# Optimization experiments

Measured on AMD Instinct MI355X. Metric: run time of the kernel, lower is better.

## Reference

```python
import jax, jax.numpy as jnp
import numpy as np

CONF_THRES = 0.25
IOU_THRES = 0.45
MAX_DET = 300
MAX_WH = 4096.0  # class offset for class-aware (non-agnostic) NMS
B, N, NC = 16, 25200, 80


def setup_inputs() -> dict:
    key = jax.random.key(0)
    k1, k2 = jax.random.split(key)
    p = jax.random.uniform(k1, (B, N, 5 + NC), dtype=jnp.float32)
    # scale to realistic YOLO pixel-space xywh for a 640x640 image
    cx = p[..., 0] * 640.0
    cy = p[..., 1] * 640.0
    w = p[..., 2] * 96.0 + 4.0
    h = p[..., 3] * 96.0 + 4.0
    obj = p[..., 4]
    cls = p[..., 5:] * 0.9
    prediction = jnp.concatenate([jnp.stack([cx, cy, w, h, obj], axis=-1), cls], axis=-1)
    logits = jax.random.normal(k2, (B, N, NC), dtype=jnp.float32)
    return {"prediction": prediction, "logits": logits}


def xywh2xyxy(b):
    cx, cy, w, h = b[..., 0], b[..., 1], b[..., 2], b[..., 3]
    return jnp.stack([cx - w * 0.5, cy - h * 0.5, cx + w * 0.5, cy + h * 0.5], axis=-1)


def _iou_one_vs_all(box, boxes):
    # box: [4], boxes: [N,4] in xyxy
    lt = jnp.maximum(box[:2], boxes[:, :2])
    rb = jnp.minimum(box[2:], boxes[:, 2:])
    wh = jnp.clip(rb - lt, 0.0)
    inter = wh[:, 0] * wh[:, 1]
    a1 = (box[2] - box[0]) * (box[3] - box[1])
    a2 = (boxes[:, 2] - boxes[:, 0]) * (boxes[:, 3] - boxes[:, 1])
    return inter / (a1 + a2 - inter + 1e-9)


def _nms_image(x6, boxes_off, scores, log_):
    # greedy NMS, fixed MAX_DET iterations; suppressed/invalid scores are -1
    def step(s, _):
        best = jnp.argmax(s)
        keep = s[best] > 0.0
        iou = _iou_one_vs_all(boxes_off[best], boxes_off)
        s = jnp.where(iou > IOU_THRES, -1.0, s)  # also suppresses 'best' (IoU=1)
        return s, (best, keep)
    _, (idx, keep) = jax.lax.scan(step, scores, None, length=MAX_DET)
    km = keep.astype(x6.dtype)[:, None]
    dets = x6[idx] * km          # [MAX_DET, 6] zero-padded
    lg = log_[idx] * km          # [MAX_DET, 80]
    return dets, lg, keep


def reference(prediction, logits):
    obj = prediction[..., 4]                          # [B,N]
    cls_conf = prediction[..., 5:] * obj[..., None]   # x[:,5:] *= x[:,4:5]
    conf = jnp.max(cls_conf, axis=-1)                 # best class conf
    j = jnp.argmax(cls_conf, axis=-1)                 # best class index
    box = xywh2xyxy(prediction[..., :4])              # [B,N,4]
    valid = (obj > CONF_THRES) & (conf > CONF_THRES)
    scores = jnp.where(valid, conf, -1.0)
    boxes_off = box + (j.astype(box.dtype) * MAX_WH)[..., None]  # class-aware offset
    x6 = jnp.concatenate([box, conf[..., None], j.astype(box.dtype)[..., None]], axis=-1)
    dets, lg, keep = jax.vmap(_nms_image)(x6, boxes_off, scores, logits)
    return dets, lg, keep
```

## Files before the change

### kernel.cpp

```cpp
#include <hip/hip_runtime.h>
#include <cstdint>

#define BB 16
#define NN 25200
#define NCLS 80
#define ROW 85
#define MAXDET 300
#define HBINS 2048
#define CAP2 512
#define TGT 448
#define CONF_T 0.25f
#define IOU_T 0.45f
#define NT 1024

static const size_t OFF_SCR = 6451200;
static const size_t OFF_CLS = 8064000;

__global__ __launch_bounds__(64) void k_pre(const float* __restrict__ pred,
                                            float4* __restrict__ boxArr,
                                            float* __restrict__ scoreArr,
                                            unsigned* __restrict__ clsArr) {
    __shared__ float tile[64 * 85];
    int lane = threadIdx.x;
    int rowbase = blockIdx.x * 64;
    const float4* src = (const float4*)(pred + (size_t)rowbase * ROW);
    float4 r[21];
#pragma unroll
    for (int it = 0; it < 21; ++it) r[it] = src[it * 64 + lane];
    float tailv = pred[(size_t)rowbase * ROW + 5376 + lane];
#pragma unroll
    for (int it = 0; it < 21; ++it) *(float4*)&tile[(it * 64 + lane) * 4] = r[it];
    tile[5376 + lane] = tailv;
    __syncthreads();

    const float* row = &tile[lane * ROW];
    float cx = row[0], cy = row[1], w = row[2], h = row[3], obj = row[4];
    float best = __fmul_rn(row[5], obj);
    int bj = 0;
#pragma unroll 4
    for (int c = 1; c < NCLS; ++c) {
        float v = __fmul_rn(row[5 + c], obj);
        if (v > best) { best = v; bj = c; }
    }
    float hw = __fmul_rn(w, 0.5f), hh = __fmul_rn(h, 0.5f);
    float4 bx;
    bx.x = __fsub_rn(cx, hw);
    bx.y = __fsub_rn(cy, hh);
    bx.z = __fadd_rn(cx, hw);
    bx.w = __fadd_rn(cy, hh);
    bool valid = (obj > CONF_T) && (best > CONF_T);

    int i = rowbase + lane;
    boxArr[i] = bx;
    scoreArr[i] = valid ? best : -1.0f;
    clsArr[i] = (unsigned)bj;
}

__global__ __launch_bounds__(NT) void k_nms(const float4* __restrict__ boxArr,
                                            const unsigned* __restrict__ clsArr,
                                            const float* __restrict__ logits,
                                            const float* __restrict__ scoreArr,
                                            float* __restrict__ out) {
    __shared__ __align__(16) char smem[63792];
    float*    ls    = (float*)smem;
    int*      li    = (int*)(smem + 2048);
    int*      flags = (int*)(smem + 4096);
    unsigned* hist  = (unsigned*)(smem + 4112);
    unsigned* csum  = (unsigned*)(smem + 12304);
    unsigned long long* mask = (unsigned long long*)(smem + 4112);
    float4*   cbox  = (float4*)(smem + 36880);
    float4*   rawbox= (float4*)(smem + 45072);
    unsigned* ccls  = (unsigned*)(smem + 53264);
    float4*   rowbox= (float4*)(smem + 55312);
    float*    rowscore = (float*)(smem + 60112);
    unsigned* rowcls   = (unsigned*)(smem + 61312);
    unsigned long long* keepm = (unsigned long long*)(smem + 62512);
    unsigned* rowsrc   = (unsigned*)(smem + 62576);

    int b = blockIdx.x, tid = threadIdx.x;

    for (int k = tid; k < HBINS; k += NT) hist[k] = 0u;
    if (tid == 0) { flags[0] = 0; flags[1] = 0; }
    __syncthreads();

    float sreg[25];
#pragma unroll
    for (int t = 0; t < 25; ++t) {
        int n = tid + t * NT;
        float s = (n < NN) ? scoreArr[(size_t)b * NN + n] : -1.0f;
        sreg[t] = s;
        if (s > 0.0f) {
            unsigned key = (__float_as_uint(s) - 0x3E800000u) >> 13;
            if (key > HBINS - 1) key = HBINS - 1;
            atomicAdd(&hist[key], 1u);
        }
    }
    __syncthreads();

    if (tid < 256) {
        unsigned cs = 0;
#pragma unroll
        for (int t = 0; t < 8; ++t) cs += hist[tid * 8 + t];
        csum[tid] = cs;
    }
    __syncthreads();
    for (int off = 1; off < 256; off <<= 1) {
        unsigned v = 0, add = 0;
        if (tid < 256) {
            v = csum[tid];
            add = (tid + off < 256) ? csum[tid + off] : 0u;
        }
        __syncthreads();
        if (tid < 256) csum[tid] = v + add;
        __syncthreads();
    }
    if (tid < 256) {
        unsigned Sc = csum[tid];
        unsigned Sn = (tid < 255) ? csum[tid + 1] : 0u;
        if (Sc >= TGT && (tid == 255 || Sn < TGT)) {
            unsigned cum = Sn;
            int t = tid * 8;
            for (int k = tid * 8 + 7; k >= tid * 8; --k) {
                cum += hist[k];
                if (cum >= TGT) { t = k; break; }
            }
            flags[1] = t;
        }
    }
    __syncthreads();
    unsigned thr = (unsigned)flags[1];

#pragma unroll
    for (int t = 0; t < 25; ++t) {
        float s = sreg[t];
        if (s > 0.0f) {
            unsigned key = (__float_as_uint(s) - 0x3E800000u) >> 13;
            if (key > HBINS - 1) key = HBINS - 1;
            if (key >= thr) {
                int pos = atomicAdd(&flags[0], 1);
                if (pos < CAP2) { ls[pos] = s; li[pos] = tid + t * NT; }
            }
        }
    }
    __syncthreads();
    int c = min(flags[0], CAP2);
    for (int p = tid; p < CAP2; p += NT)
        if (p >= c) { ls[p] = -1e30f; li[p] = 0x7fffffff; }
    __syncthreads();

    for (int k = 2; k <= CAP2; k <<= 1) {
        for (int j = k >> 1; j > 0; j >>= 1) {
            for (int i = tid; i < CAP2; i += NT) {
                int ixj = i ^ j;
                if (ixj > i) {
                    float s1 = ls[i], s2 = ls[ixj];
                    int i1 = li[i], i2 = li[ixj];
                    bool before = (s1 > s2) || (s1 == s2 && i1 < i2);
                    bool sw = ((i & k) == 0) ? !before : before;
                    if (sw) { ls[i] = s2; ls[ixj] = s1; li[i] = i2; li[ixj] = i1; }
                }
            }
            __syncthreads();
        }
    }

    for (int p = tid; p < CAP2; p += NT) {
        if (p < c) {
            int n = li[p];
            float4 bb = boxArr[(size_t)b * NN + n];
            unsigned cl = clsArr[(size_t)b * NN + n];
            rawbox[p] = bb;
            float off = __fmul_rn((float)cl, 4096.0f);
            float4 ob;
            ob.x = __fadd_rn(bb.x, off);
            ob.y = __fadd_rn(bb.y, off);
            ob.z = __fadd_rn(bb.z, off);
            ob.w = __fadd_rn(bb.w, off);
            cbox[p] = ob;
            ccls[p] = cl;
        } else {
            rawbox[p] = make_float4(0.f, 0.f, 0.f, 0.f);
            cbox[p]   = make_float4(0.f, 0.f, 0.f, 0.f);
            ccls[p] = 0u;
        }
    }
    __syncthreads();

    for (int task = tid; task < CAP2 * 8; task += NT) {
        int i = task & (CAP2 - 1);
        int w = task >> 9;
        unsigned long long m = 0ULL;
        if (i < c) {
            float4 ci = cbox[i];
            float a1 = __fmul_rn(__fsub_rn(ci.z, ci.x), __fsub_rn(ci.w, ci.y));
#pragma unroll 4
            for (int jj = 0; jj < 64; ++jj) {
                float4 cj = cbox[w * 64 + jj];
                float ltx = fmaxf(ci.x, cj.x), lty = fmaxf(ci.y, cj.y);
                float rbx = fminf(ci.z, cj.z), rby = fminf(ci.w, cj.w);
                float ww = fmaxf(__fsub_rn(rbx, ltx), 0.0f);
                float hh = fmaxf(__fsub_rn(rby, lty), 0.0f);
                float inter = __fmul_rn(ww, hh);
                if (inter > 0.0f) {
                    float a2 = __fmul_rn(__fsub_rn(cj.z, cj.x), __fsub_rn(cj.w, cj.y));
                    float denom = __fadd_rn(__fsub_rn(__fadd_rn(a1, a2), inter), 1e-9f);
                    if (inter / denom > IOU_T) m |= (1ULL << jj);
                }
            }
        }
        mask[i * 8 + w] = m;
    }
    __syncthreads();

    if (tid < 64) {
        unsigned long long rem[8] = {0,0,0,0,0,0,0,0};
        unsigned long long kp[8]  = {0,0,0,0,0,0,0,0};
        int kept = 0;
        for (int p = 0; p < c && kept < MAXDET; ++p) {
            int w = p >> 6, bit = p & 63;
            if (!((rem[w] >> bit) & 1ULL)) {
                kp[w] |= (1ULL << bit);
                kept++;
#pragma unroll
                for (int q = 0; q < 8; ++q) rem[q] |= mask[p * 8 + q];
            }
        }
        if (tid == 0) {
            flags[2] = kept;
#pragma unroll
            for (int q = 0; q < 8; ++q) keepm[q] = kp[q];
        }
    }
    __syncthreads();
    int kept = flags[2];

    {
        unsigned long long km[8];
#pragma unroll
        for (int q = 0; q < 8; ++q) km[q] = keepm[q];
        for (int p = tid; p < c; p += NT) {
            int w = p >> 6, bit = p & 63;
            if ((km[w] >> bit) & 1ULL) {
                int rank = __popcll(km[w] & ((1ULL << bit) - 1ULL));
#pragma unroll
                for (int q = 0; q < 8; ++q) rank += (q < w) ? __popcll(km[q]) : 0;
                if (rank < MAXDET) {
                    rowbox[rank] = rawbox[p];
                    rowscore[rank] = ls[p];
                    rowcls[rank] = ccls[p];
                    rowsrc[rank] = (unsigned)li[p];
                }
            }
        }
    }
    __syncthreads();

    float* dets = out;
    float* lg   = out + (size_t)BB * MAXDET * 6;
    float* kpo  = lg  + (size_t)BB * MAXDET * NCLS;

    for (int i = tid; i < MAXDET * 6; i += NT) {
        int t = i / 6, col = i - t * 6;
        float v = 0.0f;
        if (t < kept) {
            if (col < 4)      v = ((const float*)&rowbox[t])[col];
            else if (col == 4) v = rowscore[t];
            else               v = (float)rowcls[t];
        }
        dets[(size_t)b * MAXDET * 6 + i] = v;
    }
    for (int i = tid; i < MAXDET; i += NT)
        kpo[b * MAXDET + i] = (i < kept) ? 1.0f : 0.0f;
    for (int i = tid; i < MAXDET * NCLS; i += NT) {
        int t = i / NCLS, col = i - t * NCLS;
        float v = 0.0f;
        if (t < kept) v = logits[((size_t)b * NN + rowsrc[t]) * NCLS + col];
        lg[(size_t)b * MAXDET * NCLS + i] = v;
    }
}

extern "C" void kernel_launch(void* const* d_in, const int* in_sizes, int n_in,
                              void* d_out, int out_size, void* d_ws, size_t ws_size,
                              hipStream_t stream) {
    const float* pred   = (const float*)d_in[0];
    const float* logits = (const float*)d_in[1];
    float* out = (float*)d_out;
    char* ws = (char*)d_ws;

    float4*   box = (float4*)ws;
    float*    scr = (float*)(ws + OFF_SCR);
    unsigned* cls = (unsigned*)(ws + OFF_CLS);

    int blocks = (BB * NN) / 64;
    k_pre<<<blocks, 64, 0, stream>>>(pred, box, scr, cls);
    k_nms<<<BB, NT, 0, stream>>>(box, cls, logits, scr, out);
}
```

Measured before the change: 353.3 us.

## Use wave-per-row preprocessing, packed 64-bit sort keys and upper-triangle IoU masks

The preprocessing kernel changes from one thread per row with an LDS tile to one wavefront per row in a grid-stride loop. The class argmax is done with shuffles and ballot, and only lane 0 stores the results. The NMS kernel drops to 512 threads, rereads scores from global instead of holding them in registers, and packs score and inverted index into one 64-bit key so the bitonic sort moves single words. IoU mask work is limited to j>i, and the greedy suppression pass spreads the remove bitmask across lanes with shuffles. The per-row wave reads only 85 floats with 64 lanes, so much of each wave sits idle, and the half-size NMS block lowers parallelism in a single-block-per-image kernel.

```diff
diff --git a/kernel.cpp b/kernel.cpp
--- a/kernel.cpp
+++ b/kernel.cpp
@@ -11,49 +11,43 @@
 #define TGT 448
 #define CONF_T 0.25f
 #define IOU_T 0.45f
-#define NT 1024
+#define NT 512
 
 static const size_t OFF_SCR = 6451200;
 static const size_t OFF_CLS = 8064000;
 
-__global__ __launch_bounds__(64) void k_pre(const float* __restrict__ pred,
-                                            float4* __restrict__ boxArr,
-                                            float* __restrict__ scoreArr,
-                                            unsigned* __restrict__ clsArr) {
-    __shared__ float tile[64 * 85];
-    int lane = threadIdx.x;
-    int rowbase = blockIdx.x * 64;
-    const float4* src = (const float4*)(pred + (size_t)rowbase * ROW);
-    float4 r[21];
-#pragma unroll
-    for (int it = 0; it < 21; ++it) r[it] = src[it * 64 + lane];
-    float tailv = pred[(size_t)rowbase * ROW + 5376 + lane];
-#pragma unroll
-    for (int it = 0; it < 21; ++it) *(float4*)&tile[(it * 64 + lane) * 4] = r[it];
-    tile[5376 + lane] = tailv;
-    __syncthreads();
-
-    const float* row = &tile[lane * ROW];
-    float cx = row[0], cy = row[1], w = row[2], h = row[3], obj = row[4];
-    float best = __fmul_rn(row[5], obj);
-    int bj = 0;
-#pragma unroll 4
-    for (int c = 1; c < NCLS; ++c) {
-        float v = __fmul_rn(row[5 + c], obj);
-        if (v > best) { best = v; bj = c; }
-    }
-    float hw = __fmul_rn(w, 0.5f), hh = __fmul_rn(h, 0.5f);
-    float4 bx;
-    bx.x = __fsub_rn(cx, hw);
-    bx.y = __fsub_rn(cy, hh);
-    bx.z = __fadd_rn(cx, hw);
-    bx.w = __fadd_rn(cy, hh);
-    bool valid = (obj > CONF_T) && (best > CONF_T);
-
-    int i = rowbase + lane;
-    boxArr[i] = bx;
-    scoreArr[i] = valid ? best : -1.0f;
-    clsArr[i] = (unsigned)bj;
+__global__ __launch_bounds__(256) void k_pre(const float* __restrict__ pred,
+                                             float4* __restrict__ boxArr,
+                                             float* __restrict__ scoreArr,
+                                             unsigned* __restrict__ clsArr) {
+    int lane = threadIdx.x & 63;
+    int gw = blockIdx.x * 4 + (threadIdx.x >> 6);
+    int nw = gridDim.x * 4;
+    for (int row = gw; row < BB * NN; row += nw) {
+        const float* rp = pred + (size_t)row * ROW;
+        float v0 = rp[lane];
+        float v1 = (lane < 21) ? rp[64 + lane] : 0.0f;
+        float obj = __shfl(v0, 4);
+        float c0 = (lane >= 5) ? __fmul_rn(v0, obj) : -1.0f;
+        float c1 = (lane < 21) ? __fmul_rn(v1, obj) : -1.0f;
+        float mx = fmaxf(c0, c1);
+        for (int d = 1; d < 64; d <<= 1)
+            mx = fmaxf(mx, __shfl_xor(mx, d));
+        unsigned long long m0 = __ballot(c0 == mx);
+        unsigned long long m1 = __ballot(c1 == mx);
+        int bj = m0 ? (__ffsll(m0) - 6) : (__ffsll(m1) + 58);
+        float cx = __shfl(v0, 0), cy = __shfl(v0, 1);
+        float w  = __shfl(v0, 2), h  = __shfl(v0, 3);
+        if (lane == 0) {
+            float hw = __fmul_rn(w, 0.5f), hh = __fmul_rn(h, 0.5f);
+            float4 bx = make_float4(__fsub_rn(cx, hw), __fsub_rn(cy, hh),
+                                    __fadd_rn(cx, hw), __fadd_rn(cy, hh));
+            bool valid = (obj > CONF_T) && (mx > CONF_T);
+            boxArr[row] = bx;
+            scoreArr[row] = valid ? mx : -1.0f;
+            clsArr[row] = (unsigned)bj;
+        }
+    }
 }
 
 __global__ __launch_bounds__(NT) void k_nms(const float4* __restrict__ boxArr,
@@ -61,21 +55,20 @@
                                             const float* __restrict__ logits,
                                             const float* __restrict__ scoreArr,
                                             float* __restrict__ out) {
-    __shared__ __align__(16) char smem[63792];
-    float*    ls    = (float*)smem;
-    int*      li    = (int*)(smem + 2048);
-    int*      flags = (int*)(smem + 4096);
-    unsigned* hist  = (unsigned*)(smem + 4112);
-    unsigned* csum  = (unsigned*)(smem + 12304);
-    unsigned long long* mask = (unsigned long long*)(smem + 4112);
-    float4*   cbox  = (float4*)(smem + 36880);
-    float4*   rawbox= (float4*)(smem + 45072);
-    unsigned* ccls  = (unsigned*)(smem + 53264);
-    float4*   rowbox= (float4*)(smem + 55312);
-    float*    rowscore = (float*)(smem + 60112);
-    unsigned* rowcls   = (unsigned*)(smem + 61312);
-    unsigned long long* keepm = (unsigned long long*)(smem + 62512);
-    unsigned* rowsrc   = (unsigned*)(smem + 62576);
+    __shared__ __align__(16) char smem[63776];
+    unsigned* hist = (unsigned*)smem;
+    unsigned* csum = (unsigned*)(smem + 8192);
+    unsigned long long* mask = (unsigned long long*)smem;
+    unsigned long long* keys = (unsigned long long*)(smem + 32768);
+    float4*   cbox   = (float4*)(smem + 36864);
+    float4*   rawbox = (float4*)(smem + 45056);
+    unsigned* ccls   = (unsigned*)(smem + 53248);
+    float4*   rowbox = (float4*)(smem + 55296);
+    float*    rowscore = (float*)(smem + 60096);
+    unsigned* rowcls = (unsigned*)(smem + 61296);
+    unsigned* rowsrc = (unsigned*)(smem + 62496);
+    unsigned long long* keepm = (unsigned long long*)(smem + 63696);
+    int*      flags  = (int*)(smem + 63760);
 
     int b = blockIdx.x, tid = threadIdx.x;
 
@@ -83,12 +76,8 @@
     if (tid == 0) { flags[0] = 0; flags[1] = 0; }
     __syncthreads();
 
-    float sreg[25];
-#pragma unroll
-    for (int t = 0; t < 25; ++t) {
-        int n = tid + t * NT;
-        float s = (n < NN) ? scoreArr[(size_t)b * NN + n] : -1.0f;
-        sreg[t] = s;
+    for (int n = tid; n < NN; n += NT) {
+        float s = scoreArr[(size_t)b * NN + n];
         if (s > 0.0f) {
             unsigned key = (__float_as_uint(s) - 0x3E800000u) >> 13;
             if (key > HBINS - 1) key = HBINS - 1;
@@ -130,22 +119,23 @@
     __syncthreads();
     unsigned thr = (unsigned)flags[1];
 
-#pragma unroll
-    for (int t = 0; t < 25; ++t) {
-        float s = sreg[t];
+    for (int n = tid; n < NN; n += NT) {
+        float s = scoreArr[(size_t)b * NN + n];
         if (s > 0.0f) {
             unsigned key = (__float_as_uint(s) - 0x3E800000u) >> 13;
             if (key > HBINS - 1) key = HBINS - 1;
             if (key >= thr) {
                 int pos = atomicAdd(&flags[0], 1);
-                if (pos < CAP2) { ls[pos] = s; li[pos] = tid + t * NT; }
+                if (pos < CAP2)
+                    keys[pos] = ((unsigned long long)__float_as_uint(s) << 32)
+                              | (unsigned long long)(0xFFFFFFFFu - (unsigned)n);
             }
         }
     }
     __syncthreads();
     int c = min(flags[0], CAP2);
     for (int p = tid; p < CAP2; p += NT)
-        if (p >= c) { ls[p] = -1e30f; li[p] = 0x7fffffff; }
+        if (p >= c) keys[p] = 0ULL;
     __syncthreads();
 
     for (int k = 2; k <= CAP2; k <<= 1) {
@@ -153,11 +143,9 @@
             for (int i = tid; i < CAP2; i += NT) {
                 int ixj = i ^ j;
                 if (ixj > i) {
-                    float s1 = ls[i], s2 = ls[ixj];
-                    int i1 = li[i], i2 = li[ixj];
-                    bool before = (s1 > s2) || (s1 == s2 && i1 < i2);
-                    bool sw = ((i & k) == 0) ? !before : before;
-                    if (sw) { ls[i] = s2; ls[ixj] = s1; li[i] = i2; li[ixj] = i1; }
+                    unsigned long long k1 = keys[i], k2 = keys[ixj];
+                    bool sw = ((i & k) == 0) ? (k1 < k2) : (k1 > k2);
+                    if (sw) { keys[i] = k2; keys[ixj] = k1; }
                 }
             }
             __syncthreads();
@@ -166,17 +154,13 @@
 
     for (int p = tid; p < CAP2; p += NT) {
         if (p < c) {
-            int n = li[p];
+            int n = (int)(0xFFFFFFFFu - (unsigned)keys[p]);
             float4 bb = boxArr[(size_t)b * NN + n];
             unsigned cl = clsArr[(size_t)b * NN + n];
             rawbox[p] = bb;
             float off = __fmul_rn((float)cl, 4096.0f);
-            float4 ob;
-            ob.x = __fadd_rn(bb.x, off);
-            ob.y = __fadd_rn(bb.y, off);
-            ob.z = __fadd_rn(bb.z, off);
-            ob.w = __fadd_rn(bb.w, off);
-            cbox[p] = ob;
+            cbox[p] = make_float4(__fadd_rn(bb.x, off), __fadd_rn(bb.y, off),
+                                  __fadd_rn(bb.z, off), __fadd_rn(bb.w, off));
             ccls[p] = cl;
         } else {
             rawbox[p] = make_float4(0.f, 0.f, 0.f, 0.f);
@@ -189,19 +173,21 @@
     for (int task = tid; task < CAP2 * 8; task += NT) {
         int i = task & (CAP2 - 1);
         int w = task >> 9;
+        int jbase = w << 6;
         unsigned long long m = 0ULL;
-        if (i < c) {
+        if (i < c && jbase + 63 > i) {
             float4 ci = cbox[i];
             float a1 = __fmul_rn(__fsub_rn(ci.z, ci.x), __fsub_rn(ci.w, ci.y));
 #pragma unroll 4
             for (int jj = 0; jj < 64; ++jj) {
-                float4 cj = cbox[w * 64 + jj];
+                int j = jbase + jj;
+                float4 cj = cbox[j];
                 float ltx = fmaxf(ci.x, cj.x), lty = fmaxf(ci.y, cj.y);
                 float rbx = fminf(ci.z, cj.z), rby = fminf(ci.w, cj.w);
                 float ww = fmaxf(__fsub_rn(rbx, ltx), 0.0f);
                 float hh = fmaxf(__fsub_rn(rby, lty), 0.0f);
                 float inter = __fmul_rn(ww, hh);
-                if (inter > 0.0f) {
+                if (j > i && inter > 0.0f) {
                     float a2 = __fmul_rn(__fsub_rn(cj.z, cj.x), __fsub_rn(cj.w, cj.y));
                     float denom = __fadd_rn(__fsub_rn(__fadd_rn(a1, a2), inter), 1e-9f);
                     if (inter / denom > IOU_T) m |= (1ULL << jj);
@@ -213,43 +199,36 @@
     __syncthreads();
 
     if (tid < 64) {
-        unsigned long long rem[8] = {0,0,0,0,0,0,0,0};
-        unsigned long long kp[8]  = {0,0,0,0,0,0,0,0};
+        int lane = tid;
+        unsigned long long remq = 0ULL, kpq = 0ULL;
         int kept = 0;
         for (int p = 0; p < c && kept < MAXDET; ++p) {
-            int w = p >> 6, bit = p & 63;
-            if (!((rem[w] >> bit) & 1ULL)) {
-                kp[w] |= (1ULL << bit);
+            int w = p >> 6, bitp = p & 63;
+            unsigned long long tw = __shfl(remq, w);
+            if (!((tw >> bitp) & 1ULL)) {
+                if (lane < 8) remq |= mask[p * 8 + lane];
+                if (lane == w) kpq |= (1ULL << bitp);
                 kept++;
+            }
+        }
+        if (lane < 8) keepm[lane] = kpq;
+        if (lane == 0) flags[2] = kept;
+    }
+    __syncthreads();
+    int kept = flags[2];
+
+    for (int p = tid; p < c; p += NT) {
+        int w = p >> 6, bitp = p & 63;
+        unsigned long long kw = keepm[w];
+        if ((kw >> bitp) & 1ULL) {
+            int rank = __popcll(kw & ((1ULL << bitp) - 1ULL));
 #pragma unroll
-                for (int q = 0; q < 8; ++q) rem[q] |= mask[p * 8 + q];
-            }
-        }
-        if (tid == 0) {
-            flags[2] = kept;
-#pragma unroll
-            for (int q = 0; q < 8; ++q) keepm[q] = kp[q];
-        }
-    }
-    __syncthreads();
-    int kept = flags[2];
-
-    {
-        unsigned long long km[8];
-#pragma unroll
-        for (int q = 0; q < 8; ++q) km[q] = keepm[q];
-        for (int p = tid; p < c; p += NT) {
-            int w = p >> 6, bit = p & 63;
-            if ((km[w] >> bit) & 1ULL) {
-                int rank = __popcll(km[w] & ((1ULL << bit) - 1ULL));
-#pragma unroll
-                for (int q = 0; q < 8; ++q) rank += (q < w) ? __popcll(km[q]) : 0;
-                if (rank < MAXDET) {
-                    rowbox[rank] = rawbox[p];
-                    rowscore[rank] = ls[p];
-                    rowcls[rank] = ccls[p];
-                    rowsrc[rank] = (unsigned)li[p];
-                }
+            for (int q = 0; q < 8; ++q) rank += (q < w) ? __popcll(keepm[q]) : 0;
+            if (rank < MAXDET) {
+                rowbox[rank] = rawbox[p];
+                rowscore[rank] = __uint_as_float((unsigned)(keys[p] >> 32));
+                rowcls[rank] = ccls[p];
+                rowsrc[rank] = 0xFFFFFFFFu - (unsigned)keys[p];
             }
         }
     }
@@ -263,7 +242,7 @@
         int t = i / 6, col = i - t * 6;
         float v = 0.0f;
         if (t < kept) {
-            if (col < 4)      v = ((const float*)&rowbox[t])[col];
+            if (col < 4)       v = ((const float*)&rowbox[t])[col];
             else if (col == 4) v = rowscore[t];
             else               v = (float)rowcls[t];
         }
@@ -291,7 +270,6 @@
     float*    scr = (float*)(ws + OFF_SCR);
     unsigned* cls = (unsigned*)(ws + OFF_CLS);
 
-    int blocks = (BB * NN) / 64;
-    k_pre<<<blocks, 64, 0, stream>>>(pred, box, scr, cls);
+    k_pre<<<2520, 256, 0, stream>>>(pred, box, scr, cls);
     k_nms<<<BB, NT, 0, stream>>>(box, cls, logits, scr, out);
 }
```

Result: slower. 426.4 us (+20.7%).
